# Optimization experiments

Measured on AMD Instinct MI355X. Metric: run time of the kernel, lower is better.

Reference implementation:

```python
import jax, jax.numpy as jnp
import numpy as np

N, M, D, H = 16, 1024, 64, 4  # batch, num_node, dim_in==dim_hid, num_head
NEG_SLOPE = 0.2


def setup_inputs() -> dict:
    key = jax.random.key(0)
    ks = jax.random.split(key, 10)
    s = 1.0 / np.sqrt(D)
    inp = {
        "x": jax.random.normal(ks[0], (N, M, D), dtype=jnp.float32),
        "edge": jnp.zeros((N, M, M), dtype=jnp.float32),  # unused by the module
        # stacked per-head Linear(dim_in, dim_hid) params: weight (H, D_out, D_in), bias (H, D_out)
        "Wk": (jax.random.normal(ks[1], (H, D, D), dtype=jnp.float32) * s),
        "bk": (jax.random.normal(ks[2], (H, D), dtype=jnp.float32) * s),
        "Wq": (jax.random.normal(ks[3], (H, D, D), dtype=jnp.float32) * s),
        "bq": (jax.random.normal(ks[4], (H, D), dtype=jnp.float32) * s),
        "Wv": (jax.random.normal(ks[5], (H, D, D), dtype=jnp.float32) * s),
        "bv": (jax.random.normal(ks[6], (H, D), dtype=jnp.float32) * s),
        # decoder: Linear(dim_hid*num_head -> dim_in)
        "Wdec": (jax.random.normal(ks[7], (D, H * D), dtype=jnp.float32) / np.sqrt(H * D)),
        "bdec": (jax.random.normal(ks[8], (D,), dtype=jnp.float32) / np.sqrt(H * D)),
    }
    return inp


def reference(x, edge, Wk, bk, Wq, bq, Wv, bv, Wdec, bdec):
    # x: (N, M, D). Per head h: K = x @ Wk[h].T + bk[h], etc.
    K = jnp.einsum("nmd,hed->nhme", x, Wk) + bk[None, :, None, :]  # (N,H,M,D)
    Q = jnp.einsum("nmd,hed->nhme", x, Wq) + bq[None, :, None, :]
    V = jnp.einsum("nmd,hed->nhme", x, Wv) + bv[None, :, None, :]
    # alpha[n,h,i,j] = K[n,h,i] . Q[n,h,j]  (sender=K row i, receiver=Q row j)
    alpha = jnp.einsum("nhie,nhje->nhij", K, Q)  # (N,H,M,M)
    alpha = jax.nn.leaky_relu(alpha, NEG_SLOPE)
    alpha = jax.nn.softmax(alpha, axis=-1)
    agg = jnp.einsum("nhij,nhje->nhie", alpha, V)  # (N,H,M,D)
    dx = jax.nn.leaky_relu(agg, NEG_SLOPE) - x[:, None, :, :]  # (N,H,M,D)
    # concat heads along feature dim (head 0 first): (N, M, H*D)
    dx = dx.transpose(0, 2, 1, 3).reshape(N, M, H * D)
    return dx @ Wdec.T + bdec  # (N, M, D)
```

## Files before the change

kernel.cpp:

```cpp
#include <hip/hip_runtime.h>
#include <hip/hip_bf16.h>


#define NB 16
#define MM 1024
#define DD 64
#define HH 4
#define NEG 0.2f
#define AST 72
#define DST 264

typedef __attribute__((ext_vector_type(8))) short bf16x8;
typedef __attribute__((ext_vector_type(8))) _Float16 f16x8;
typedef __attribute__((ext_vector_type(16))) float f32x16;

__device__ inline unsigned short f2bf(float f) {
  unsigned int u = __builtin_bit_cast(unsigned int, f);
  unsigned int r = (u + 0x7FFFu + ((u >> 16) & 1u)) >> 16;
  return (unsigned short)r;
}
__device__ inline unsigned short f2h(float f) {
  _Float16 h = (_Float16)f;
  return __builtin_bit_cast(unsigned short, h);
}

__global__ __launch_bounds__(256) void prep_kernel(
    const float* __restrict__ Wk, const float* __restrict__ Wq,
    const float* __restrict__ Wv, const float* __restrict__ Wdec,
    unsigned short* __restrict__ Wf) {
  const int idx = (blockIdx.x * 256 + threadIdx.x) * 4;
  const int seg = idx >> 14, local = idx & 16383;
  const float* src = seg == 0 ? Wk : seg == 1 ? Wq : seg == 2 ? Wv : Wdec;
  float4 v = *(const float4*)&src[local];
  unsigned short p[4] = {f2h(v.x), f2h(v.y), f2h(v.z), f2h(v.w)};
  *(uint2*)&Wf[idx] = *(uint2*)p;
}

__global__ __launch_bounds__(256) void proj_kernel(
    const float* __restrict__ x, const unsigned short* __restrict__ Wf,
    const float* __restrict__ bk, const float* __restrict__ bq, const float* __restrict__ bv,
    unsigned short* __restrict__ Kf, unsigned short* __restrict__ Qf,
    unsigned short* __restrict__ Vtg) {
  __shared__ unsigned short xs[64 * AST];
  __shared__ unsigned short ob[64 * AST];
  const int t = threadIdx.x;
  const int r0 = blockIdx.x * 64;
  const int combo = blockIdx.y, mat = combo >> 2, h = combo & 3;
  const int n = r0 >> 10, ml = r0 & 1023;
  const float* bias = mat == 0 ? bk : (mat == 1 ? bq : bv);

#pragma unroll
  for (int rep = 0; rep < 2; ++rep) {
    int idx = rep * 256 + t, row = idx >> 3, c8 = (idx & 7) * 8;
    float4 a = *(const float4*)&x[(size_t)(r0 + row) * DD + c8];
    float4 b = *(const float4*)&x[(size_t)(r0 + row) * DD + c8 + 4];
    unsigned short p[8] = {f2h(a.x), f2h(a.y), f2h(a.z), f2h(a.w),
                           f2h(b.x), f2h(b.y), f2h(b.z), f2h(b.w)};
    *(uint4*)&xs[row * AST + c8] = *(uint4*)p;
  }
  __syncthreads();

  const int w = t >> 6, lane = t & 63, m31 = lane & 31, hf = lane >> 5;
  const int mi = w >> 1, ne = w & 1;
  const int ecol = h * 64 + ne * 32 + m31;
  const float bb = bias[ecol];

  f32x16 C;
#pragma unroll
  for (int r = 0; r < 16; ++r) C[r] = 0.f;
#pragma unroll
  for (int ks = 0; ks < 4; ++ks) {
    f16x8 xa = *(f16x8*)&xs[(mi * 32 + m31) * AST + ks * 16 + hf * 8];
    f16x8 wb = *(const f16x8*)&Wf[(size_t)mat * 16384 + (size_t)ecol * DD + ks * 16 + hf * 8];
    C = __builtin_amdgcn_mfma_f32_32x32x16_f16(xa, wb, C, 0, 0, 0);
  }

  if (mat < 2) {
#pragma unroll
    for (int r = 0; r < 16; ++r) {
      int rr = (r & 3) + 8 * (r >> 2) + 4 * hf;
      ob[(mi * 32 + rr) * AST + ne * 32 + m31] = f2h(C[r] + bb);
    }
  } else {
#pragma unroll
    for (int r = 0; r < 16; ++r) {
      int rr = (r & 3) + 8 * (r >> 2) + 4 * hf;
      ob[(ne * 32 + m31) * AST + mi * 32 + rr] = f2bf(C[r] + bb);
    }
  }
  __syncthreads();

  if (mat < 2) {
    unsigned short* dst = mat == 0 ? Kf : Qf;
    const size_t obase = (((size_t)n * HH + h) * MM + ml) * DD;
#pragma unroll
    for (int rep = 0; rep < 2; ++rep) {
      int idx = rep * 256 + t, row = idx >> 3, c8 = (idx & 7) * 8;
      *(uint4*)&dst[obase + (size_t)row * DD + c8] = *(uint4*)&ob[row * AST + c8];
    }
  } else {
    const size_t obase = (((size_t)n * HH + h) * DD) * MM + ml;
#pragma unroll
    for (int rep = 0; rep < 2; ++rep) {
      int idx = rep * 256 + t, row = idx >> 3, c8 = (idx & 7) * 8;
      *(uint4*)&Vtg[obase + (size_t)row * MM + c8] = *(uint4*)&ob[row * AST + c8];
    }
  }
}

__global__ __launch_bounds__(256, 4) void attn_kernel(
    const unsigned short* __restrict__ Kf, const unsigned short* __restrict__ Qf,
    const unsigned short* __restrict__ Vtg, const float* __restrict__ x,
    unsigned short* __restrict__ DX) {
  __shared__ unsigned short qh[64 * AST];
  __shared__ unsigned short vt[64 * AST];
  __shared__ unsigned short ps[64 * AST];
  __shared__ float ls[64];

  const int t = threadIdx.x;
  const int w = t >> 6, lane = t & 63;
  const int m31 = lane & 31, hf = lane >> 5;
  const int ti = w >> 1, tw = w & 1;
  const int i0 = blockIdx.x * 64, h = blockIdx.y, n = blockIdx.z;
  const size_t base = (((size_t)n * HH + h) * MM) * DD;
  const size_t baseT = (((size_t)n * HH + h) * DD) * MM;

  f16x8 kfrag[4];
#pragma unroll
  for (int ks = 0; ks < 4; ++ks)
    kfrag[ks] = *(const f16x8*)&Kf[base + (size_t)(i0 + ti * 32 + m31) * DD + ks * 16 + hf * 8];

  f32x16 agg, accl;
#pragma unroll
  for (int r = 0; r < 16; ++r) { agg[r] = 0.f; accl[r] = 0.f; }
  bf16x8 ones;
#pragma unroll
  for (int r = 0; r < 8; ++r) ones[r] = (short)0x3F80;

  for (int jt = 0; jt < 16; ++jt) {
    const int j0 = jt * 64;
    __syncthreads();
#pragma unroll
    for (int rep = 0; rep < 2; ++rep) {
      int idx = rep * 256 + t, row = idx >> 3, c8 = (idx & 7) * 8;
      *(uint4*)&qh[row * AST + c8] = *(const uint4*)&Qf[base + (size_t)(j0 + row) * DD + c8];
      *(uint4*)&vt[row * AST + c8] = *(const uint4*)&Vtg[baseT + (size_t)row * MM + j0 + c8];
    }
    __syncthreads();

    f32x16 C;
#pragma unroll
    for (int r = 0; r < 16; ++r) C[r] = 0.f;
#pragma unroll
    for (int ks = 0; ks < 4; ++ks) {
      f16x8 qf = *(f16x8*)&qh[(tw * 32 + m31) * AST + ks * 16 + hf * 8];
      C = __builtin_amdgcn_mfma_f32_32x32x16_f16(kfrag[ks], qf, C, 0, 0, 0);
    }
#pragma unroll
    for (int r = 0; r < 16; ++r) {
      float s = C[r];
      s = s > 0.f ? s : NEG * s;
      int rr = (r & 3) + 8 * (r >> 2) + 4 * hf;
      ps[(ti * 32 + rr) * AST + tw * 32 + m31] = f2bf(__expf(s));
    }
    __syncthreads();

#pragma unroll
    for (int ks = 0; ks < 4; ++ks) {
      bf16x8 aP = *(bf16x8*)&ps[(ti * 32 + m31) * AST + ks * 16 + hf * 8];
      bf16x8 bV = *(bf16x8*)&vt[(tw * 32 + m31) * AST + ks * 16 + hf * 8];
      agg = __builtin_amdgcn_mfma_f32_32x32x16_bf16(aP, bV, agg, 0, 0, 0);
      if (tw == 0)
        accl = __builtin_amdgcn_mfma_f32_32x32x16_bf16(aP, ones, accl, 0, 0, 0);
    }
  }

  if (tw == 0 && m31 == 0) {
#pragma unroll
    for (int r = 0; r < 16; ++r) {
      int rr = (r & 3) + 8 * (r >> 2) + 4 * hf;
      ls[ti * 32 + rr] = accl[r];
    }
  }
  __syncthreads();

#pragma unroll
  for (int r = 0; r < 16; ++r) {
    int rr = (r & 3) + 8 * (r >> 2) + 4 * hf;
    float l = ls[ti * 32 + rr];
    float v = agg[r] / l;
    v = v > 0.f ? v : NEG * v;
    v -= x[((size_t)n * MM + i0 + ti * 32 + rr) * DD + tw * 32 + m31];
    ps[(ti * 32 + rr) * AST + tw * 32 + m31] = f2h(v);
  }
  __syncthreads();
#pragma unroll
  for (int rep = 0; rep < 2; ++rep) {
    int idx = rep * 256 + t, row = idx >> 3, c8 = (idx & 7) * 8;
    *(uint4*)&DX[((size_t)n * MM + i0 + row) * (HH * DD) + h * DD + c8] =
        *(uint4*)&ps[row * AST + c8];
  }
}

__global__ __launch_bounds__(256) void dec_kernel(
    const unsigned short* __restrict__ DX, const unsigned short* __restrict__ Wdf,
    const float* __restrict__ bdec, float* __restrict__ out) {
  __shared__ unsigned short dxs[64 * DST];
  const int t = threadIdx.x;
  const int w = t >> 6, lane = t & 63, m31 = lane & 31, hf = lane >> 5;
  const int mi = w >> 1, nd = w & 1;
  const int r0 = blockIdx.x * 64;
#pragma unroll
  for (int rep = 0; rep < 8; ++rep) {
    int idx = rep * 256 + t, row = idx >> 5, c8 = (idx & 31) * 8;
    *(uint4*)&dxs[row * DST + c8] = *(const uint4*)&DX[(size_t)(r0 + row) * 256 + c8];
  }
  __syncthreads();
  const float bb = bdec[nd * 32 + m31];
  f32x16 C;
#pragma unroll
  for (int r = 0; r < 16; ++r) C[r] = 0.f;
#pragma unroll
  for (int ks = 0; ks < 16; ++ks) {
    f16x8 aD = *(f16x8*)&dxs[(mi * 32 + m31) * DST + ks * 16 + hf * 8];
    f16x8 bW = *(const f16x8*)&Wdf[(size_t)(nd * 32 + m31) * 256 + ks * 16 + hf * 8];
    C = __builtin_amdgcn_mfma_f32_32x32x16_f16(aD, bW, C, 0, 0, 0);
  }
#pragma unroll
  for (int r = 0; r < 16; ++r) {
    int rr = (r & 3) + 8 * (r >> 2) + 4 * hf;
    out[(size_t)(r0 + mi * 32 + rr) * DD + nd * 32 + m31] = C[r] + bb;
  }
}

extern "C" void kernel_launch(void* const* d_in, const int* in_sizes, int n_in,
                              void* d_out, int out_size, void* d_ws, size_t ws_size,
                              hipStream_t stream) {
  const float* x    = (const float*)d_in[0];
  const float* Wk   = (const float*)d_in[2];
  const float* bk   = (const float*)d_in[3];
  const float* Wq   = (const float*)d_in[4];
  const float* bq   = (const float*)d_in[5];
  const float* Wv   = (const float*)d_in[6];
  const float* bv   = (const float*)d_in[7];
  const float* Wdec = (const float*)d_in[8];
  const float* bdec = (const float*)d_in[9];
  float* out = (float*)d_out;

  const size_t seg = (size_t)NB * HH * MM * DD;
  unsigned short* Kf  = (unsigned short*)d_ws;
  unsigned short* Qf  = Kf + seg;
  unsigned short* Vt  = Qf + seg;
  unsigned short* DXp = Vt + seg;
  unsigned short* Wf  = DXp + seg;
  unsigned short* Wdf = Wf + 3 * 16384;

  prep_kernel<<<64, 256, 0, stream>>>(Wk, Wq, Wv, Wdec, Wf);
  proj_kernel<<<dim3(256, 12), 256, 0, stream>>>(x, Wf, bk, bq, bv, Kf, Qf, Vt);
  attn_kernel<<<dim3(16, HH, NB), 256, 0, stream>>>(Kf, Qf, Vt, x, DXp);
  dec_kernel<<<NB * MM / 64, 256, 0, stream>>>(DXp, Wdf, bdec, out);
}
```

Baseline: 162.2 us.

## Restructure attention kernel: register-resident P, double-buffered Q/V, exp2 and XCD-aware mapping

The attention kernel now handles 128 query rows per block, one 32-row strip per wave. The softmax probabilities stay in registers, packed with cvt_pk_bf16 and permlane32 swaps, which removes the LDS round trip for P and the extra MFMA that computed row sums. Q and V tiles are prefetched into registers and written to a double-buffered LDS region, so each iteration needs only one barrier. K is pre-scaled by log2e in the projection so exp2 can replace exp, and blocks are remapped so a head's blocks share an XCD for L2 locality. The costs are higher register pressure (launch bounds drop to 2 waves/SIMD) and fewer blocks in the grid.

Measured after the change: 149.8 us. -7.6%, faster.

```diff
diff --git a/kernel.cpp b/kernel.cpp
--- a/kernel.cpp
+++ b/kernel.cpp
@@ -9,10 +9,13 @@
 #define NEG 0.2f
 #define AST 72
 #define DST 264
+#define LOG2E 1.44269504088896f
 
 typedef __attribute__((ext_vector_type(8))) short bf16x8;
 typedef __attribute__((ext_vector_type(8))) _Float16 f16x8;
 typedef __attribute__((ext_vector_type(16))) float f32x16;
+typedef __attribute__((ext_vector_type(4))) unsigned int uint4v;
+typedef __attribute__((ext_vector_type(2))) unsigned int uint2v;
 
 __device__ inline unsigned short f2bf(float f) {
   unsigned int u = __builtin_bit_cast(unsigned int, f);
@@ -22,6 +25,16 @@
 __device__ inline unsigned short f2h(float f) {
   _Float16 h = (_Float16)f;
   return __builtin_bit_cast(unsigned short, h);
+}
+__device__ inline unsigned int pk_bf16(float lo, float hi) {
+  unsigned int r;
+  asm("v_cvt_pk_bf16_f32 %0, %1, %2" : "=v"(r) : "v"(lo), "v"(hi));
+  return r;
+}
+__device__ inline void swap32(unsigned int& a, unsigned int& b) {
+  uint2v r = __builtin_amdgcn_permlane32_swap(a, b, false, false);
+  a = r.x;
+  b = r.y;
 }
 
 __global__ __launch_bounds__(256) void prep_kernel(
@@ -76,10 +89,11 @@
   }
 
   if (mat < 2) {
+    const float ksc = (mat == 0) ? LOG2E : 1.0f;
 #pragma unroll
     for (int r = 0; r < 16; ++r) {
       int rr = (r & 3) + 8 * (r >> 2) + 4 * hf;
-      ob[(mi * 32 + rr) * AST + ne * 32 + m31] = f2h(C[r] + bb);
+      ob[(mi * 32 + rr) * AST + ne * 32 + m31] = f2h((C[r] + bb) * ksc);
     }
   } else {
 #pragma unroll
@@ -108,97 +122,149 @@
   }
 }
 
-__global__ __launch_bounds__(256, 4) void attn_kernel(
+__global__ __launch_bounds__(256, 2) void attn_kernel(
     const unsigned short* __restrict__ Kf, const unsigned short* __restrict__ Qf,
     const unsigned short* __restrict__ Vtg, const float* __restrict__ x,
     unsigned short* __restrict__ DX) {
-  __shared__ unsigned short qh[64 * AST];
-  __shared__ unsigned short vt[64 * AST];
-  __shared__ unsigned short ps[64 * AST];
-  __shared__ float ls[64];
+  __shared__ __align__(16) unsigned short sm[4 * 64 * AST];
+  __shared__ float ls[128];
 
   const int t = threadIdx.x;
   const int w = t >> 6, lane = t & 63;
   const int m31 = lane & 31, hf = lane >> 5;
-  const int ti = w >> 1, tw = w & 1;
-  const int i0 = blockIdx.x * 64, h = blockIdx.y, n = blockIdx.z;
+
+  const int slot = blockIdx.x + 8 * (blockIdx.y + HH * (int)blockIdx.z);
+  const int xcd = slot & 7, within = slot >> 3;
+  const int grp = xcd * 8 + (within >> 3);
+  const int ib = within & 7;
+  const int n = grp >> 2, h = grp & 3;
+  const int i0 = ib * 128;
+
   const size_t base = (((size_t)n * HH + h) * MM) * DD;
   const size_t baseT = (((size_t)n * HH + h) * DD) * MM;
+  const unsigned short* Qp = Qf + base;
+  const unsigned short* Vp = Vtg + baseT;
 
   f16x8 kfrag[4];
 #pragma unroll
   for (int ks = 0; ks < 4; ++ks)
-    kfrag[ks] = *(const f16x8*)&Kf[base + (size_t)(i0 + ti * 32 + m31) * DD + ks * 16 + hf * 8];
-
-  f32x16 agg, accl;
-#pragma unroll
-  for (int r = 0; r < 16; ++r) { agg[r] = 0.f; accl[r] = 0.f; }
-  bf16x8 ones;
-#pragma unroll
-  for (int r = 0; r < 8; ++r) ones[r] = (short)0x3F80;
-
+    kfrag[ks] = *(const f16x8*)&Kf[base + (size_t)(i0 + w * 32 + m31) * DD + ks * 16 + hf * 8];
+
+  const int r0 = t >> 3, c8 = (t & 7) * 8;
+
+  {
+    uint4 qa = *(const uint4*)&Qp[(size_t)r0 * DD + c8];
+    uint4 qb2 = *(const uint4*)&Qp[(size_t)(r0 + 32) * DD + c8];
+    uint4 va = *(const uint4*)&Vp[(size_t)r0 * MM + c8];
+    uint4 vb2 = *(const uint4*)&Vp[(size_t)(r0 + 32) * MM + c8];
+    *(uint4*)&sm[r0 * AST + c8] = qa;
+    *(uint4*)&sm[(r0 + 32) * AST + c8] = qb2;
+    unsigned short* vb0 = sm + 2 * 64 * AST;
+    *(uint4*)&vb0[r0 * AST + c8] = va;
+    *(uint4*)&vb0[(r0 + 32) * AST + c8] = vb2;
+  }
+  __syncthreads();
+
+  f32x16 agg0, agg1;
+#pragma unroll
+  for (int r = 0; r < 16; ++r) { agg0[r] = 0.f; agg1[r] = 0.f; }
+  float lac = 0.f;
+
+  uint4 qrA, qrB, vrA, vrB;
+
+#pragma unroll 2
   for (int jt = 0; jt < 16; ++jt) {
-    const int j0 = jt * 64;
+    unsigned short* qb = sm + (jt & 1) * (64 * AST);
+    unsigned short* vb = sm + (2 + (jt & 1)) * (64 * AST);
+
+    if (jt < 15) {
+      const int j0n = (jt + 1) * 64;
+      qrA = *(const uint4*)&Qp[(size_t)(j0n + r0) * DD + c8];
+      qrB = *(const uint4*)&Qp[(size_t)(j0n + r0 + 32) * DD + c8];
+      vrA = *(const uint4*)&Vp[(size_t)r0 * MM + j0n + c8];
+      vrB = *(const uint4*)&Vp[(size_t)(r0 + 32) * MM + j0n + c8];
+    }
+
+    bf16x8 pa[4];
+#pragma unroll
+    for (int tile = 0; tile < 2; ++tile) {
+      f32x16 C;
+#pragma unroll
+      for (int r = 0; r < 16; ++r) C[r] = 0.f;
+#pragma unroll
+      for (int ks = 0; ks < 4; ++ks) {
+        f16x8 qa = *(f16x8*)&qb[(tile * 32 + m31) * AST + ks * 16 + hf * 8];
+        C = __builtin_amdgcn_mfma_f32_32x32x16_f16(qa, kfrag[ks], C, 0, 0, 0);
+      }
+#pragma unroll
+      for (int r = 0; r < 16; ++r) {
+        float s = C[r];
+        s = fmaxf(s, NEG * s);
+        s = __builtin_amdgcn_exp2f(s);
+        lac += s;
+        C[r] = s;
+      }
+      {
+        unsigned int p01 = pk_bf16(C[0], C[1]), p23 = pk_bf16(C[2], C[3]);
+        unsigned int p45 = pk_bf16(C[4], C[5]), p67 = pk_bf16(C[6], C[7]);
+        swap32(p01, p45);
+        swap32(p23, p67);
+        uint4v wlo = {p01, p23, p45, p67};
+        pa[2 * tile] = __builtin_bit_cast(bf16x8, wlo);
+      }
+      {
+        unsigned int p89 = pk_bf16(C[8], C[9]), pAB = pk_bf16(C[10], C[11]);
+        unsigned int pCD = pk_bf16(C[12], C[13]), pEF = pk_bf16(C[14], C[15]);
+        swap32(p89, pCD);
+        swap32(pAB, pEF);
+        uint4v whi = {p89, pAB, pCD, pEF};
+        pa[2 * tile + 1] = __builtin_bit_cast(bf16x8, whi);
+      }
+    }
+
+#pragma unroll
+    for (int ks = 0; ks < 4; ++ks) {
+      bf16x8 bv0 = *(bf16x8*)&vb[m31 * AST + ks * 16 + hf * 8];
+      bf16x8 bv1 = *(bf16x8*)&vb[(32 + m31) * AST + ks * 16 + hf * 8];
+      agg0 = __builtin_amdgcn_mfma_f32_32x32x16_bf16(pa[ks], bv0, agg0, 0, 0, 0);
+      agg1 = __builtin_amdgcn_mfma_f32_32x32x16_bf16(pa[ks], bv1, agg1, 0, 0, 0);
+    }
+
+    if (jt < 15) {
+      unsigned short* qn = sm + ((jt & 1) ^ 1) * (64 * AST);
+      unsigned short* vn = sm + (2 + ((jt & 1) ^ 1)) * (64 * AST);
+      *(uint4*)&qn[r0 * AST + c8] = qrA;
+      *(uint4*)&qn[(r0 + 32) * AST + c8] = qrB;
+      *(uint4*)&vn[r0 * AST + c8] = vrA;
+      *(uint4*)&vn[(r0 + 32) * AST + c8] = vrB;
+    }
     __syncthreads();
-#pragma unroll
-    for (int rep = 0; rep < 2; ++rep) {
-      int idx = rep * 256 + t, row = idx >> 3, c8 = (idx & 7) * 8;
-      *(uint4*)&qh[row * AST + c8] = *(const uint4*)&Qf[base + (size_t)(j0 + row) * DD + c8];
-      *(uint4*)&vt[row * AST + c8] = *(const uint4*)&Vtg[baseT + (size_t)row * MM + j0 + c8];
-    }
-    __syncthreads();
-
-    f32x16 C;
-#pragma unroll
-    for (int r = 0; r < 16; ++r) C[r] = 0.f;
-#pragma unroll
-    for (int ks = 0; ks < 4; ++ks) {
-      f16x8 qf = *(f16x8*)&qh[(tw * 32 + m31) * AST + ks * 16 + hf * 8];
-      C = __builtin_amdgcn_mfma_f32_32x32x16_f16(kfrag[ks], qf, C, 0, 0, 0);
-    }
-#pragma unroll
-    for (int r = 0; r < 16; ++r) {
-      float s = C[r];
-      s = s > 0.f ? s : NEG * s;
-      int rr = (r & 3) + 8 * (r >> 2) + 4 * hf;
-      ps[(ti * 32 + rr) * AST + tw * 32 + m31] = f2bf(__expf(s));
-    }
-    __syncthreads();
-
-#pragma unroll
-    for (int ks = 0; ks < 4; ++ks) {
-      bf16x8 aP = *(bf16x8*)&ps[(ti * 32 + m31) * AST + ks * 16 + hf * 8];
-      bf16x8 bV = *(bf16x8*)&vt[(tw * 32 + m31) * AST + ks * 16 + hf * 8];
-      agg = __builtin_amdgcn_mfma_f32_32x32x16_bf16(aP, bV, agg, 0, 0, 0);
-      if (tw == 0)
-        accl = __builtin_amdgcn_mfma_f32_32x32x16_bf16(aP, ones, accl, 0, 0, 0);
-    }
-  }
-
-  if (tw == 0 && m31 == 0) {
-#pragma unroll
-    for (int r = 0; r < 16; ++r) {
-      int rr = (r & 3) + 8 * (r >> 2) + 4 * hf;
-      ls[ti * 32 + rr] = accl[r];
-    }
-  }
+  }
+
+  const float lsum = lac + __shfl_xor(lac, 32);
+  if (hf == 0) ls[w * 32 + m31] = lsum;
   __syncthreads();
 
 #pragma unroll
   for (int r = 0; r < 16; ++r) {
-    int rr = (r & 3) + 8 * (r >> 2) + 4 * hf;
-    float l = ls[ti * 32 + rr];
-    float v = agg[r] / l;
-    v = v > 0.f ? v : NEG * v;
-    v -= x[((size_t)n * MM + i0 + ti * 32 + rr) * DD + tw * 32 + m31];
-    ps[(ti * 32 + rr) * AST + tw * 32 + m31] = f2h(v);
-  }
-  __syncthreads();
-#pragma unroll
-  for (int rep = 0; rep < 2; ++rep) {
-    int idx = rep * 256 + t, row = idx >> 3, c8 = (idx & 7) * 8;
-    *(uint4*)&DX[((size_t)n * MM + i0 + row) * (HH * DD) + h * DD + c8] =
-        *(uint4*)&ps[row * AST + c8];
+    const int rr = (r & 3) + 8 * (r >> 2) + 4 * hf;
+    const float rl = 1.0f / ls[w * 32 + rr];
+    const size_t xrow = ((size_t)n * MM + i0 + w * 32 + rr) * DD;
+    float v0 = agg0[r] * rl;
+    v0 = fmaxf(v0, NEG * v0);
+    v0 -= x[xrow + m31];
+    sm[(w * 32 + rr) * AST + m31] = f2h(v0);
+    float v1 = agg1[r] * rl;
+    v1 = fmaxf(v1, NEG * v1);
+    v1 -= x[xrow + 32 + m31];
+    sm[(w * 32 + rr) * AST + 32 + m31] = f2h(v1);
+  }
+  __syncthreads();
+#pragma unroll
+  for (int rep = 0; rep < 4; ++rep) {
+    const int idx = rep * 256 + t, row = idx >> 3, cc = (idx & 7) * 8;
+    *(uint4*)&DX[((size_t)n * MM + i0 + row) * (HH * DD) + h * DD + cc] =
+        *(uint4*)&sm[row * AST + cc];
   }
 }
 
@@ -257,6 +323,6 @@
 
   prep_kernel<<<64, 256, 0, stream>>>(Wk, Wq, Wv, Wdec, Wf);
   proj_kernel<<<dim3(256, 12), 256, 0, stream>>>(x, Wf, bk, bq, bv, Kf, Qf, Vt);
-  attn_kernel<<<dim3(16, HH, NB), 256, 0, stream>>>(Kf, Qf, Vt, x, DXp);
+  attn_kernel<<<dim3(8, HH, NB), 256, 0, stream>>>(Kf, Qf, Vt, x, DXp);
   dec_kernel<<<NB * MM / 64, 256, 0, stream>>>(DXp, Wdf, bdec, out);
 }
```
